# Performance work log

Hardware: AMD Instinct MI355X
Metric: run time of the kernel (lower is better)

The kernel has to match this reference:

```python
import jax, jax.numpy as jnp
import numpy as np

N_KG, N, E, R, H, D_OUT = 50000, 20000, 320000, 8, 4, 64
IN_CH = 256  # 128 kg_emb + 128 ccle projection
HD = H * D_OUT  # 256


def setup_inputs() -> dict:
    key = jax.random.key(0)
    ks = jax.random.split(key, 16)
    nrm = lambda k, shape, s=0.05: jax.random.normal(k, shape, dtype=jnp.float32) * s
    return {
        "kg_emb": nrm(ks[0], (N_KG, 128), 1.0),
        "ccle": nrm(ks[1], (N_KG, 4), 1.0),
        "node_id": jax.random.randint(ks[2], (N,), 0, N_KG),
        "edge_index": jax.random.randint(ks[3], (2, E), 0, N),
        "edge_type": jax.random.randint(ks[4], (E,), 0, R),
        "ccle_w1": nrm(ks[5], (4, 32)), "ccle_b1": jnp.zeros((32,), jnp.float32),
        "ccle_w2": nrm(ks[6], (32, 128)), "ccle_b2": jnp.zeros((128,), jnp.float32),
        "w1": nrm(ks[7], (R, IN_CH, HD)),
        "q1": nrm(ks[8], (HD, H)), "k1": nrm(ks[9], (HD, H)),
        "bias1": jnp.zeros((HD,), jnp.float32),
        "w2": nrm(ks[10], (R, HD, HD)),
        "q2": nrm(ks[11], (HD, H)), "k2": nrm(ks[12], (HD, H)),
        "bias2": jnp.zeros((HD,), jnp.float32),
        "skip_w1": nrm(ks[13], (IN_CH, 256)), "skip_b1": jnp.zeros((256,), jnp.float32),
        "skip_w2": nrm(ks[14], (256, 256)), "skip_b2": jnp.zeros((256,), jnp.float32),
    }


def _segment_softmax(logits, segs, n):
    # numerically stable softmax over variable-size dst-neighborhoods
    m = jax.lax.stop_gradient(jax.ops.segment_max(logits, segs, num_segments=n))
    m = jnp.where(jnp.isfinite(m), m, 0.0)
    e = jnp.exp(logits - m[segs])
    s = jax.ops.segment_sum(e, segs, num_segments=n)
    return e / jnp.maximum(s[segs], 1e-16)


def _rgat(x, edge_index, edge_type, w, q, k, bias, n):
    # PyG RGATConv: additive-self-attention, across-relation, dim=1, concat=True
    # per-relation node transform then per-edge gather == x_e @ w[edge_type]
    xw = jnp.einsum('nd,rdo->rno', x, w)              # [R, N, H*D]
    src, dst = edge_index[0], edge_index[1]
    outj = xw[edge_type, src]                          # [E, H*D] source feats
    outi = xw[edge_type, dst]                          # [E, H*D] target feats
    alpha = jax.nn.leaky_relu(outi @ q + outj @ k, 0.2)  # [E, H]
    alpha = _segment_softmax(alpha, dst, n)
    msg = (outj.reshape(-1, H, D_OUT) * alpha[:, :, None]).reshape(-1, HD)
    return jax.ops.segment_sum(msg, dst, num_segments=n) + bias


def reference(kg_emb, ccle, ccle_w1, ccle_b1, ccle_w2, ccle_b2,
              w1, q1, k1, bias1, w2, q2, k2, bias2,
              skip_w1, skip_b1, skip_w2, skip_b2,
              node_id, edge_index, edge_type):
    lrelu = lambda v: jax.nn.leaky_relu(v, 0.01)  # nn.LeakyReLU default slope
    ccle_out = lrelu(ccle @ ccle_w1 + ccle_b1) @ ccle_w2 + ccle_b2
    x_in = jnp.concatenate([kg_emb[node_id], ccle_out[node_id]], axis=1)  # [N, 256]
    n = x_in.shape[0]
    x = lrelu(_rgat(x_in, edge_index, edge_type, w1, q1, k1, bias1, n))
    # dropout is identity in eval mode
    x = _rgat(x, edge_index, edge_type, w2, q2, k2, bias2, n)
    skip = lrelu(x_in @ skip_w1 + skip_b1) @ skip_w2 + skip_b2
    return lrelu(x + skip)
```

## Files before the change

### kernel.cpp

```cpp
#include <hip/hip_runtime.h>
#include <hip/hip_bf16.h>

typedef __bf16 bf16x8 __attribute__((ext_vector_type(8)));
typedef float  f32x4  __attribute__((ext_vector_type(4)));
typedef float  v2f    __attribute__((ext_vector_type(2)));

#define BUCKET 128

__device__ __forceinline__ void async_cp16(const __bf16* g, __bf16* l) {
    __builtin_amdgcn_global_load_lds(
        (const __attribute__((address_space(1))) void*)g,
        (__attribute__((address_space(3))) void*)l, 16, 0, 0);
}

__global__ __launch_bounds__(256) void preamble_kernel(
    const float* __restrict__ kg_emb, const float* __restrict__ ccle,
    const float* __restrict__ cw1, const float* __restrict__ cb1,
    const float* __restrict__ cw2, const float* __restrict__ cb2,
    const int* __restrict__ node_id, __bf16* __restrict__ x_in, int Nn,
    const float* __restrict__ w1, const float* __restrict__ w2,
    const float* __restrict__ sw1, const float* __restrict__ sw2,
    __bf16* __restrict__ w1t, __bf16* __restrict__ w2t,
    __bf16* __restrict__ sw1t, __bf16* __restrict__ sw2t, int R,
    const float* __restrict__ q1, const float* __restrict__ k1,
    const float* __restrict__ q2, const float* __restrict__ k2,
    __bf16* __restrict__ wqkT1, __bf16* __restrict__ wqkT2,
    const int* __restrict__ ei, const int* __restrict__ et,
    int* __restrict__ cnt, int* __restrict__ cidx, int E,
    int nTrans, int nWqk, int nBx)
{
    __shared__ __align__(16) char sraw[8448];
    const int bid = blockIdx.x;
    const int t = threadIdx.x;

    if (bid < nTrans) {
        __bf16 (*tile)[65] = (__bf16 (*)[65])sraw;
        int zr = bid >> 4, rem = bid & 15;
        int kb = (rem & 3) * 64, nb = (rem >> 2) * 64;
        const float* B; __bf16* Bt;
        if (zr < R)           { B = w1 + (size_t)zr * 65536;       Bt = w1t + (size_t)zr * 65536; }
        else if (zr < 2 * R)  { B = w2 + (size_t)(zr - R) * 65536; Bt = w2t + (size_t)(zr - R) * 65536; }
        else if (zr == 2 * R) { B = sw1;                            Bt = sw1t; }
        else                  { B = sw2;                            Bt = sw2t; }
        for (int idx = t; idx < 4096; idx += 256) {
            int rr = idx >> 6, cc = idx & 63;
            tile[rr][cc] = (__bf16)B[(kb + rr) * 256 + nb + cc];
        }
        __syncthreads();
        for (int idx = t; idx < 4096; idx += 256) {
            int rr = idx >> 6, cc = idx & 63;
            Bt[(nb + rr) * 256 + kb + cc] = tile[cc][rr];
        }
    } else if (bid < nTrans + nWqk) {
        float* qs = (float*)sraw;
        float* ks = qs + 1024;
        int wb = bid - nTrans;
        int zz = wb >> 3, ib = wb & 7;
        int r = zz % R;
        const float* w = (zz < R) ? w1 : w2;
        const float* q = (zz < R) ? q1 : q2;
        const float* k = (zz < R) ? k1 : k2;
        __bf16* wqkT = (zz < R) ? wqkT1 : wqkT2;
        for (int i = t; i < 1024; i += 256) { qs[i] = q[i]; ks[i] = k[i]; }
        __syncthreads();
        int inl = t >> 3, g = t & 7;
        const float* wr = w + (size_t)r * 65536;
        int in = ib * 32 + inl;
        float pq0=0,pq1=0,pq2=0,pq3=0, pk0=0,pk1=0,pk2=0,pk3=0;
        const float* row = wr + in * 256 + g * 32;
        #pragma unroll 8
        for (int oj = 0; oj < 32; oj++) {
            float wv = row[oj];
            int out = g * 32 + oj;
            pq0 += wv * qs[out*4+0]; pq1 += wv * qs[out*4+1];
            pq2 += wv * qs[out*4+2]; pq3 += wv * qs[out*4+3];
            pk0 += wv * ks[out*4+0]; pk1 += wv * ks[out*4+1];
            pk2 += wv * ks[out*4+2]; pk3 += wv * ks[out*4+3];
        }
        #pragma unroll
        for (int d = 4; d >= 1; d >>= 1) {
            pq0 += __shfl_down(pq0, d, 64); pq1 += __shfl_down(pq1, d, 64);
            pq2 += __shfl_down(pq2, d, 64); pq3 += __shfl_down(pq3, d, 64);
            pk0 += __shfl_down(pk0, d, 64); pk1 += __shfl_down(pk1, d, 64);
            pk2 += __shfl_down(pk2, d, 64); pk3 += __shfl_down(pk3, d, 64);
        }
        if (g == 0) {
            wqkT[(r*8+0)*256 + in] = (__bf16)pq0; wqkT[(r*8+1)*256 + in] = (__bf16)pq1;
            wqkT[(r*8+2)*256 + in] = (__bf16)pq2; wqkT[(r*8+3)*256 + in] = (__bf16)pq3;
            wqkT[(r*8+4)*256 + in] = (__bf16)pk0; wqkT[(r*8+5)*256 + in] = (__bf16)pk1;
            wqkT[(r*8+6)*256 + in] = (__bf16)pk2; wqkT[(r*8+7)*256 + in] = (__bf16)pk3;
        }
    } else if (bid < nTrans + nWqk + nBx) {
        float (*h)[32] = (float (*)[32])sraw;
        int bb = bid - nTrans - nWqk;
        int sub = t >> 7;
        int tt  = t & 127;
        int i   = bb * 2 + sub;
        if (i < Nn && tt < 32) {
            int kid = node_id[i];
            float a = 0.f;
            #pragma unroll
            for (int j = 0; j < 4; j++) a += ccle[kid*4 + j] * cw1[j*32 + tt];
            a += cb1[tt];
            h[sub][tt] = a < 0.f ? 0.01f * a : a;
        }
        __syncthreads();
        if (i < Nn) {
            int kid = node_id[i];
            x_in[i*256 + tt] = (__bf16)kg_emb[kid*128 + tt];
            float a = 0.f;
            #pragma unroll
            for (int j = 0; j < 32; j++) a += h[sub][j] * cw2[j*128 + tt];
            a += cb2[tt];
            x_in[i*256 + 128 + tt] = (__bf16)a;
        }
    } else {
        int e = (bid - nTrans - nWqk - nBx) * 256 + t;
        if (e < E) {
            int d = ei[E + e];
            int pos = atomicAdd(&cnt[d], 1);
            if (pos < BUCKET) cidx[(long)d * BUCKET + pos] = (et[e] << 20) | ei[e];
        }
    }
}

__global__ __launch_bounds__(256, 3) void gemm_lds_kernel(
    const __bf16* __restrict__ A, const __bf16* __restrict__ Askip,
    const __bf16* __restrict__ Bt, long bStride, const __bf16* __restrict__ Bskip,
    const __bf16* __restrict__ wqkT,
    unsigned char* __restrict__ C8, long cStride,
    __bf16* __restrict__ Cskip, const float* __restrict__ biasSkip, float slopeSkip,
    float* __restrict__ s_qk,
    int M, int R2, int mb, int nMem, int hasSkip)
{
    __shared__ __bf16 sm[2][8192];
    const int id = blockIdx.x;
    const int xcd = id & 7, slot = id >> 3;
    const int g = xcd + 8 * (slot / nMem);
    const int member = slot % nMem;
    if (g >= mb) return;
    const bool isSqk  = (member == nMem - 1);
    const bool isSkip = hasSkip && !isSqk && (member >= R2);
    const int m0 = g * 128;
    const int n0 = isSkip ? (member - R2) * 128 : ((member < R2) ? (member & 1) * 128 : 0);
    const int z = (member < R2) ? (member >> 1) : 0;
    const __bf16* __restrict__ Ab = isSkip ? Askip : A;
    const __bf16* __restrict__ Bb = isSqk ? wqkT : (isSkip ? Bskip : (Bt + (long)z * bStride));

    const int t = threadIdx.x;
    const int wave = t >> 6, lane = t & 63;
    const int wy = (wave >> 1) * 64, wx = (wave & 1) * 64;
    const int lr = lane & 15, lq = lane >> 4;

    int c0 = wave * 128 + lane;
    int row0 = c0 >> 2, kq0 = ((c0 & 3) ^ ((row0 >> 1) & 3));
    int c1 = c0 + 64;
    int row1 = c1 >> 2, kq1 = ((c1 & 3) ^ ((row1 >> 1) & 3));
    int ar0 = m0 + row0; if (ar0 >= M) ar0 = M - 1;
    int ar1 = m0 + row1; if (ar1 >= M) ar1 = M - 1;
    const long a_g0 = (long)ar0 * 256 + kq0 * 8;
    const long a_g1 = (long)ar1 * 256 + kq1 * 8;
    const long b_g0 = (long)(n0 + row0) * 256 + kq0 * 8;
    const long b_g1 = (long)(n0 + row1) * 256 + kq1 * 8;
    const int lds_w0 = (wave * 128) * 8, lds_w1 = (wave * 128 + 64) * 8;

    int a_lds[4], b_lds[4];
    #pragma unroll
    for (int tm = 0; tm < 4; tm++) {
        int row = wy + tm * 16 + lr;
        a_lds[tm] = (row * 4 + (lq ^ ((row >> 1) & 3))) * 8;
    }
    #pragma unroll
    for (int tn = 0; tn < 4; tn++) {
        int row = wx + tn * 16 + lr;
        b_lds[tn] = 4096 + (row * 4 + (lq ^ ((row >> 1) & 3))) * 8;
    }

    f32x4 acc[4][4];
    #pragma unroll
    for (int a_ = 0; a_ < 4; a_++)
        #pragma unroll
        for (int b_ = 0; b_ < 4; b_++) acc[a_][b_] = (f32x4){0.f, 0.f, 0.f, 0.f};

    async_cp16(Ab + a_g0, &sm[0][lds_w0]);
    async_cp16(Ab + a_g1, &sm[0][lds_w1]);
    async_cp16(Bb + b_g0, &sm[0][4096 + lds_w0]);
    async_cp16(Bb + b_g1, &sm[0][4096 + lds_w1]);

    #pragma unroll
    for (int it = 0; it < 8; it++) {
        const int cur = it & 1;
        __syncthreads();
        if (it < 7) {
            const int k0 = (it + 1) * 32;
            async_cp16(Ab + a_g0 + k0, &sm[cur ^ 1][lds_w0]);
            async_cp16(Ab + a_g1 + k0, &sm[cur ^ 1][lds_w1]);
            async_cp16(Bb + b_g0 + k0, &sm[cur ^ 1][4096 + lds_w0]);
            async_cp16(Bb + b_g1 + k0, &sm[cur ^ 1][4096 + lds_w1]);
        }
        bf16x8 af[4], bfr[4];
        #pragma unroll
        for (int tm = 0; tm < 4; tm++) af[tm]  = *(const bf16x8*)(&sm[cur][a_lds[tm]]);
        #pragma unroll
        for (int tn = 0; tn < 4; tn++) bfr[tn] = *(const bf16x8*)(&sm[cur][b_lds[tn]]);
        #pragma unroll
        for (int tm = 0; tm < 4; tm++)
            #pragma unroll
            for (int tn = 0; tn < 4; tn++)
                acc[tm][tn] = __builtin_amdgcn_mfma_f32_16x16x32_bf16(af[tm], bfr[tn], acc[tm][tn], 0, 0, 0);
    }

    if (isSqk) {
        if (wx == 0) {
            #pragma unroll
            for (int tm = 0; tm < 4; tm++) {
                #pragma unroll
                for (int tn = 0; tn < 4; tn++) {
                    int col = tn * 16 + lr;
                    #pragma unroll
                    for (int ii = 0; ii < 4; ii++) {
                        int rg = m0 + wy + tm * 16 + lq * 4 + ii;
                        if (rg < M) s_qk[(long)rg * 64 + col] = acc[tm][tn][ii];
                    }
                }
            }
        }
    } else if (isSkip) {
        #pragma unroll
        for (int tm = 0; tm < 4; tm++) {
            #pragma unroll
            for (int tn = 0; tn < 4; tn++) {
                int col = n0 + wx + tn * 16 + lr;
                float bcol = biasSkip[col];
                #pragma unroll
                for (int ii = 0; ii < 4; ii++) {
                    int rg = m0 + wy + tm * 16 + lq * 4 + ii;
                    if (rg < M) {
                        float v = acc[tm][tn][ii] + bcol;
                        v = v < 0.f ? v * slopeSkip : v;
                        Cskip[(long)rg * 256 + col] = (__bf16)v;
                    }
                }
            }
        }
    } else {
        unsigned char* __restrict__ Cb = C8 + (long)z * cStride;
        #pragma unroll
        for (int tm = 0; tm < 4; tm++) {
            #pragma unroll
            for (int tn = 0; tn < 4; tn++) {
                int col = n0 + wx + tn * 16 + lr;
                #pragma unroll
                for (int ii = 0; ii < 4; ii++) {
                    int rg = m0 + wy + tm * 16 + lq * 4 + ii;
                    if (rg < M) {
                        float v = acc[tm][tn][ii];
                        int pk = __builtin_amdgcn_cvt_pk_fp8_f32(v, v, 0, false);
                        Cb[(long)rg * 256 + col] = (unsigned char)(pk & 0xFF);
                    }
                }
            }
        }
    }
}

__global__ __launch_bounds__(256) void agg_skip_kernel(
    const unsigned char* __restrict__ XW8, const float* __restrict__ s_qk,
    const int* __restrict__ degArr, const int* __restrict__ cidx,
    const float* __restrict__ bias, __bf16* __restrict__ outb, float slope, int Nn,
    const __bf16* __restrict__ Ask, const __bf16* __restrict__ Bsk,
    __bf16* __restrict__ Csk, const float* __restrict__ biasSk, int nSkip)
{
    extern __shared__ __bf16 smx[];
    if ((int)blockIdx.x < nSkip) {
        const int sb = blockIdx.x;
        const int m0 = (sb >> 1) * 128;
        const int n0 = (sb & 1) * 128;
        const int t = threadIdx.x;
        const int wave = t >> 6, lane = t & 63;
        const int wy = (wave >> 1) * 64, wx = (wave & 1) * 64;
        const int lr = lane & 15, lq = lane >> 4;

        int c0 = wave * 128 + lane;
        int row0 = c0 >> 2, kq0 = ((c0 & 3) ^ ((row0 >> 1) & 3));
        int c1 = c0 + 64;
        int row1 = c1 >> 2, kq1 = ((c1 & 3) ^ ((row1 >> 1) & 3));
        int ar0 = m0 + row0; if (ar0 >= Nn) ar0 = Nn - 1;
        int ar1 = m0 + row1; if (ar1 >= Nn) ar1 = Nn - 1;
        const long a_g0 = (long)ar0 * 256 + kq0 * 8;
        const long a_g1 = (long)ar1 * 256 + kq1 * 8;
        const long b_g0 = (long)(n0 + row0) * 256 + kq0 * 8;
        const long b_g1 = (long)(n0 + row1) * 256 + kq1 * 8;
        const int lds_w0 = (wave * 128) * 8, lds_w1 = (wave * 128 + 64) * 8;

        int a_lds[4], b_lds[4];
        #pragma unroll
        for (int tm = 0; tm < 4; tm++) {
            int row = wy + tm * 16 + lr;
            a_lds[tm] = (row * 4 + (lq ^ ((row >> 1) & 3))) * 8;
        }
        #pragma unroll
        for (int tn = 0; tn < 4; tn++) {
            int row = wx + tn * 16 + lr;
            b_lds[tn] = 4096 + (row * 4 + (lq ^ ((row >> 1) & 3))) * 8;
        }

        f32x4 acc[4][4];
        #pragma unroll
        for (int a_ = 0; a_ < 4; a_++)
            #pragma unroll
            for (int b_ = 0; b_ < 4; b_++) acc[a_][b_] = (f32x4){0.f, 0.f, 0.f, 0.f};

        async_cp16(Ask + a_g0, &smx[lds_w0]);
        async_cp16(Ask + a_g1, &smx[lds_w1]);
        async_cp16(Bsk + b_g0, &smx[4096 + lds_w0]);
        async_cp16(Bsk + b_g1, &smx[4096 + lds_w1]);

        #pragma unroll
        for (int it = 0; it < 8; it++) {
            const int cur = it & 1;
            __syncthreads();
            if (it < 7) {
                const int k0 = (it + 1) * 32;
                async_cp16(Ask + a_g0 + k0, &smx[(cur ^ 1) * 8192 + lds_w0]);
                async_cp16(Ask + a_g1 + k0, &smx[(cur ^ 1) * 8192 + lds_w1]);
                async_cp16(Bsk + b_g0 + k0, &smx[(cur ^ 1) * 8192 + 4096 + lds_w0]);
                async_cp16(Bsk + b_g1 + k0, &smx[(cur ^ 1) * 8192 + 4096 + lds_w1]);
            }
            bf16x8 af[4], bfr[4];
            #pragma unroll
            for (int tm = 0; tm < 4; tm++) af[tm]  = *(const bf16x8*)(&smx[cur * 8192 + a_lds[tm]]);
            #pragma unroll
            for (int tn = 0; tn < 4; tn++) bfr[tn] = *(const bf16x8*)(&smx[cur * 8192 + b_lds[tn]]);
            #pragma unroll
            for (int tm = 0; tm < 4; tm++)
                #pragma unroll
                for (int tn = 0; tn < 4; tn++)
                    acc[tm][tn] = __builtin_amdgcn_mfma_f32_16x16x32_bf16(af[tm], bfr[tn], acc[tm][tn], 0, 0, 0);
        }

        #pragma unroll
        for (int tm = 0; tm < 4; tm++) {
            #pragma unroll
            for (int tn = 0; tn < 4; tn++) {
                int col = n0 + wx + tn * 16 + lr;
                float bcol = biasSk[col];
                #pragma unroll
                for (int ii = 0; ii < 4; ii++) {
                    int rg = m0 + wy + tm * 16 + lq * 4 + ii;
                    if (rg < Nn) Csk[(long)rg * 256 + col] = (__bf16)(acc[tm][tn][ii] + bcol);
                }
            }
        }
        return;
    }

    int* cc_l   = (int*)smx;
    float* p_l  = (float*)((char*)smx + 1024);
    int w = threadIdx.x >> 6;
    int lane = threadIdx.x & 63;
    int i = ((int)blockIdx.x - nSkip) * 4 + w;
    if (i >= Nn) return;
    long base = (long)i * BUCKET;
    int deg = degArr[i]; if (deg > BUCKET) deg = BUCKET;

    int half = lane >> 5;
    int l32 = lane & 31;
    int myh = l32 >> 3;
    int d8 = l32 * 8;

    float4 bv0 = *(const float4*)(bias + d8);
    float4 bv1 = *(const float4*)(bias + d8 + 4);

    float acc[8];
    #pragma unroll
    for (int u = 0; u < 8; u++) acc[u] = 0.f;
    float ss0 = 0.f, ss1 = 0.f, ss2 = 0.f, ss3 = 0.f;

    for (int c0 = 0; c0 < deg; c0 += 64) {
        int e = c0 + lane;
        int cc = 0;
        if (e < deg) cc = cidx[base + e];
        cc_l[w * 64 + lane] = cc;
        int cnt = min(64, deg - c0);

        uint2 xv[8];
        #pragma unroll
        for (int u = 0; u < 8; u++) {
            int cj = cc_l[w * 64 + u * 2 + half];
            int src = cj & 0xFFFFF, et = cj >> 20;
            xv[u] = *(const uint2*)(XW8 + ((long)et * Nn + src) * 256 + d8);
        }

        float p0 = 0.f, p1 = 0.f, p2 = 0.f, p3 = 0.f;
        if (e < deg) {
            int src = cc & 0xFFFFF, et = cc >> 20;
            float4 sqv = *(const float4*)(s_qk + (long)i * 64 + et * 8);
            float4 skv = *(const float4*)(s_qk + (long)src * 64 + et * 8 + 4);
            float l0 = sqv.x + skv.x; l0 = l0 < 0.f ? 0.2f * l0 : l0;
            float l1 = sqv.y + skv.y; l1 = l1 < 0.f ? 0.2f * l1 : l1;
            float l2 = sqv.z + skv.z; l2 = l2 < 0.f ? 0.2f * l2 : l2;
            float l3 = sqv.w + skv.w; l3 = l3 < 0.f ? 0.2f * l3 : l3;
            p0 = __expf(fminf(l0, 40.f)); p1 = __expf(fminf(l1, 40.f));
            p2 = __expf(fminf(l2, 40.f)); p3 = __expf(fminf(l3, 40.f));
        }
// ... 17 lines not shown
            #pragma unroll
            for (int u = 0; u < 8; u++) {
                int srcl = j0 + u * 2 + half;
                float wgt = p_l[(w * 4 + myh) * 64 + srcl];
                uint2 xvu = xv[u];
                v2f f0 = __builtin_amdgcn_cvt_pk_f32_fp8(xvu.x, false);
                v2f f1 = __builtin_amdgcn_cvt_pk_f32_fp8(xvu.x, true);
                v2f f2 = __builtin_amdgcn_cvt_pk_f32_fp8(xvu.y, false);
                v2f f3 = __builtin_amdgcn_cvt_pk_f32_fp8(xvu.y, true);
                acc[0] += wgt * f0.x; acc[1] += wgt * f0.y;
                acc[2] += wgt * f1.x; acc[3] += wgt * f1.y;
                acc[4] += wgt * f2.x; acc[5] += wgt * f2.y;
                acc[6] += wgt * f3.x; acc[7] += wgt * f3.y;
            }
            if (more) {
                #pragma unroll
                for (int u = 0; u < 8; u++) xv[u] = xvn[u];
            }
        }
    }
    #pragma unroll
    for (int u = 0; u < 8; u++) acc[u] += __shfl_xor(acc[u], 32, 64);
    #pragma unroll
    for (int off = 32; off >= 1; off >>= 1) {
        ss0 += __shfl_xor(ss0, off, 64);
        ss1 += __shfl_xor(ss1, off, 64);
        ss2 += __shfl_xor(ss2, off, 64);
        ss3 += __shfl_xor(ss3, off, 64);
    }
    float ssh = (myh & 2) ? ((myh & 1) ? ss3 : ss2) : ((myh & 1) ? ss1 : ss0);
    float inv = 1.f / fmaxf(ssh, 1e-16f);

    float barr[8] = { bv0.x, bv0.y, bv0.z, bv0.w, bv1.x, bv1.y, bv1.z, bv1.w };
    if (half == 0) {
        __bf16 tmp[8];
        #pragma unroll
        for (int u = 0; u < 8; u++) {
            float v = acc[u] * inv + barr[u];
            tmp[u] = (__bf16)(v < 0.f ? slope * v : v);
        }
        *(uint4*)(outb + (long)i * 256 + d8) = *(const uint4*)tmp;
    }
}

__global__ __launch_bounds__(256) void agg_kernel(
    const unsigned char* __restrict__ XW8, const float* __restrict__ s_qk,
    const int* __restrict__ degArr, const int* __restrict__ cidx,
    const float* __restrict__ bias, const __bf16* __restrict__ skipb,
    __bf16* __restrict__ outb, float* __restrict__ outf, float slope, int Nn)
{
    __shared__ int   cc_s[4][64];
    __shared__ float p_s[4][4][64];
    int w = threadIdx.x >> 6;
    int lane = threadIdx.x & 63;
    int i = blockIdx.x * 4 + w;
    if (i >= Nn) return;
    long base = (long)i * BUCKET;
    int deg = degArr[i]; if (deg > BUCKET) deg = BUCKET;

    int half = lane >> 5;
    int l32 = lane & 31;
    int myh = l32 >> 3;
    int d8 = l32 * 8;

    float4 bv0 = *(const float4*)(bias + d8);
    float4 bv1 = *(const float4*)(bias + d8 + 4);
    uint4 skq = make_uint4(0u, 0u, 0u, 0u);
    if (skipb) skq = *(const uint4*)(skipb + (long)i * 256 + d8);

    float acc[8];
    #pragma unroll
    for (int u = 0; u < 8; u++) acc[u] = 0.f;
    float ss0 = 0.f, ss1 = 0.f, ss2 = 0.f, ss3 = 0.f;

    for (int c0 = 0; c0 < deg; c0 += 64) {
        int e = c0 + lane;
        int cc = 0;
        if (e < deg) cc = cidx[base + e];
        cc_s[w][lane] = cc;
        int cnt = min(64, deg - c0);

        uint2 xv[8];
        #pragma unroll
        for (int u = 0; u < 8; u++) {
            int cj = cc_s[w][u * 2 + half];
            int src = cj & 0xFFFFF, et = cj >> 20;
            xv[u] = *(const uint2*)(XW8 + ((long)et * Nn + src) * 256 + d8);
        }

        float p0 = 0.f, p1 = 0.f, p2 = 0.f, p3 = 0.f;
        if (e < deg) {
            int src = cc & 0xFFFFF, et = cc >> 20;
            float4 sqv = *(const float4*)(s_qk + (long)i * 64 + et * 8);
            float4 skv = *(const float4*)(s_qk + (long)src * 64 + et * 8 + 4);
            float l0 = sqv.x + skv.x; l0 = l0 < 0.f ? 0.2f * l0 : l0;
            float l1 = sqv.y + skv.y; l1 = l1 < 0.f ? 0.2f * l1 : l1;
            float l2 = sqv.z + skv.z; l2 = l2 < 0.f ? 0.2f * l2 : l2;
            float l3 = sqv.w + skv.w; l3 = l3 < 0.f ? 0.2f * l3 : l3;
            p0 = __expf(fminf(l0, 40.f)); p1 = __expf(fminf(l1, 40.f));
            p2 = __expf(fminf(l2, 40.f)); p3 = __expf(fminf(l3, 40.f));
        }
        ss0 += p0; ss1 += p1; ss2 += p2; ss3 += p3;
        p_s[w][0][lane] = p0;
        p_s[w][1][lane] = p1;
        p_s[w][2][lane] = p2;
        p_s[w][3][lane] = p3;

        for (int j0 = 0; j0 < cnt; j0 += 16) {
            uint2 xvn[8];
            const bool more = (j0 + 16 < cnt);
            if (more) {
                #pragma unroll
                for (int u = 0; u < 8; u++) {
                    int cj = cc_s[w][j0 + 16 + u * 2 + half];
                    int src = cj & 0xFFFFF, et = cj >> 20;
                    xvn[u] = *(const uint2*)(XW8 + ((long)et * Nn + src) * 256 + d8);
                }
            }
            #pragma unroll
            for (int u = 0; u < 8; u++) {
                int srcl = j0 + u * 2 + half;
                float wgt = p_s[w][myh][srcl];
                uint2 xvu = xv[u];
                v2f f0 = __builtin_amdgcn_cvt_pk_f32_fp8(xvu.x, false);
                v2f f1 = __builtin_amdgcn_cvt_pk_f32_fp8(xvu.x, true);
                v2f f2 = __builtin_amdgcn_cvt_pk_f32_fp8(xvu.y, false);
                v2f f3 = __builtin_amdgcn_cvt_pk_f32_fp8(xvu.y, true);
                acc[0] += wgt * f0.x; acc[1] += wgt * f0.y;
                acc[2] += wgt * f1.x; acc[3] += wgt * f1.y;
                acc[4] += wgt * f2.x; acc[5] += wgt * f2.y;
                acc[6] += wgt * f3.x; acc[7] += wgt * f3.y;
            }
            if (more) {
                #pragma unroll
                for (int u = 0; u < 8; u++) xv[u] = xvn[u];
            }
        }
    }
    #pragma unroll
    for (int u = 0; u < 8; u++) acc[u] += __shfl_xor(acc[u], 32, 64);
    #pragma unroll
    for (int off = 32; off >= 1; off >>= 1) {
        ss0 += __shfl_xor(ss0, off, 64);
        ss1 += __shfl_xor(ss1, off, 64);
        ss2 += __shfl_xor(ss2, off, 64);
        ss3 += __shfl_xor(ss3, off, 64);
    }
    float ssh = (myh & 2) ? ((myh & 1) ? ss3 : ss2) : ((myh & 1) ? ss1 : ss0);
    float inv = 1.f / fmaxf(ssh, 1e-16f);

    float barr[8] = { bv0.x, bv0.y, bv0.z, bv0.w, bv1.x, bv1.y, bv1.z, bv1.w };
    const __bf16* skp = (const __bf16*)&skq;
    float vout[8];
    #pragma unroll
    for (int u = 0; u < 8; u++) {
        float v = acc[u] * inv + barr[u];
        if (skipb) v += (float)skp[u];
        vout[u] = v < 0.f ? slope * v : v;
    }
    if (outb) {
        if (half == 0) {
            __bf16 tmp[8];
            #pragma unroll
            for (int u = 0; u < 8; u++) tmp[u] = (__bf16)vout[u];
            *(uint4*)(outb + (long)i * 256 + d8) = *(const uint4*)tmp;
        }
    } else {
        float4 f4;
        if (half == 0) { f4 = make_float4(vout[0], vout[1], vout[2], vout[3]);
                         *(float4*)(outf + (long)i * 256 + d8) = f4; }
        else           { f4 = make_float4(vout[4], vout[5], vout[6], vout[7]);
                         *(float4*)(outf + (long)i * 256 + d8 + 4) = f4; }
    }
}

extern "C" void kernel_launch(void* const* d_in, const int* in_sizes, int n_in,
                              void* d_out, int out_size, void* d_ws, size_t ws_size,
                              hipStream_t stream)
{
    const float* kg_emb  = (const float*)d_in[0];
    const float* ccle    = (const float*)d_in[1];
    const int*   node_id = (const int*)d_in[2];
    const int*   edge_ix = (const int*)d_in[3];
    const int*   edge_ty = (const int*)d_in[4];
    const float* ccle_w1 = (const float*)d_in[5];
    const float* ccle_b1 = (const float*)d_in[6];
    const float* ccle_w2 = (const float*)d_in[7];
    const float* ccle_b2 = (const float*)d_in[8];
    const float* w1      = (const float*)d_in[9];
    const float* q1      = (const float*)d_in[10];
    const float* k1      = (const float*)d_in[11];
    const float* bias1   = (const float*)d_in[12];
    const float* w2      = (const float*)d_in[13];
    const float* q2      = (const float*)d_in[14];
    const float* k2      = (const float*)d_in[15];
    const float* bias2   = (const float*)d_in[16];
    const float* skip_w1 = (const float*)d_in[17];
    const float* skip_b1 = (const float*)d_in[18];
    const float* skip_w2 = (const float*)d_in[19];
    const float* skip_b2 = (const float*)d_in[20];

    const int Nn = in_sizes[2];
    const int E  = in_sizes[4];
    const int R  = in_sizes[9] / (256 * 256);

    char* p = (char*)d_ws;
    auto alloc = [&](size_t bytes) { char* r = p; p += (bytes + 255) & ~(size_t)255; return r; };
    __bf16* x_in  = (__bf16*)alloc((size_t)Nn * 256 * 2);
    __bf16* x1    = (__bf16*)alloc((size_t)Nn * 256 * 2);
    __bf16* sh    = (__bf16*)alloc((size_t)Nn * 256 * 2);
    __bf16* skipb = (__bf16*)alloc((size_t)Nn * 256 * 2);
    unsigned char* XW8 = (unsigned char*)alloc((size_t)R * Nn * 256);
    float*  s_qk  = (float*)alloc((size_t)Nn * 64 * 4);
    __bf16* wqkT1 = (__bf16*)alloc((size_t)64 * 256 * 2);
    __bf16* wqkT2 = (__bf16*)alloc((size_t)64 * 256 * 2);
    __bf16* w1t   = (__bf16*)alloc((size_t)R * 65536 * 2);
    __bf16* w2t   = (__bf16*)alloc((size_t)R * 65536 * 2);
    __bf16* sw1t  = (__bf16*)alloc((size_t)65536 * 2);
    __bf16* sw2t  = (__bf16*)alloc((size_t)65536 * 2);
    int* cnt  = (int*)alloc((size_t)Nn * 4);
    int* cidx = (int*)alloc((size_t)Nn * BUCKET * 4);

    const int mb = (Nn + 127) / 128;
    const int eb = (E + 255) / 256;
    const int grp = (mb + 7) / 8;
    const int R2 = 2 * R;
    const int gemm1_blocks = 8 * grp * (R2 + 3);
    const int gemm2_blocks = 8 * grp * (R2 + 1);

    const int nTrans = 16 * (2 * R + 2);
    const int nWqk   = 2 * R * 8;
    const int nBx    = (Nn + 1) / 2;
    const int pre_blocks = nTrans + nWqk + nBx + eb;
    const int nSkip2 = 2 * mb;

    (void)hipMemsetAsync(cnt, 0, (size_t)Nn * 4, stream);
    preamble_kernel<<<dim3(pre_blocks), 256, 0, stream>>>(
        kg_emb, ccle, ccle_w1, ccle_b1, ccle_w2, ccle_b2, node_id, x_in, Nn,
        w1, w2, skip_w1, skip_w2, w1t, w2t, sw1t, sw2t, R,
        q1, k1, q2, k2, wqkT1, wqkT2,
        edge_ix, edge_ty, cnt, cidx, E, nTrans, nWqk, nBx);

    gemm_lds_kernel<<<dim3(gemm1_blocks), 256, 0, stream>>>(
        x_in, x_in, w1t, 65536L, sw1t, wqkT1, XW8, (long)Nn * 256, sh, skip_b1, 0.01f,
        s_qk, Nn, R2, mb, R2 + 3, 1);

    agg_skip_kernel<<<dim3(nSkip2 + (Nn + 3) / 4), 256, 32768, stream>>>(
        XW8, s_qk, cnt, cidx, bias1, x1, 0.01f, Nn,
        sh, sw2t, skipb, skip_b2, nSkip2);

    gemm_lds_kernel<<<dim3(gemm2_blocks), 256, 0, stream>>>(
        x1, x1, w2t, 65536L, sw2t, wqkT2, XW8, (long)Nn * 256, skipb, skip_b2, 1.0f,
        s_qk, Nn, R2, mb, R2 + 1, 0);

    agg_kernel<<<dim3((Nn + 3) / 4), 256, 0, stream>>>(
        XW8, s_qk, cnt, cidx, bias2, skipb, nullptr, (float*)d_out, 0.01f, Nn);
}
```

Baseline: 294.5 us.

## Fuse all stages into one persistent kernel with software grid barriers

Replaces the five separate launches (preamble, two GEMMs, two aggregations) with one persistent mega-kernel. Blocks loop over job indices for each stage and are separated by atomic-counter grid barriers. This removes the launch gaps and tail idle time between stages. In exchange every stage now runs with one shared-memory size and register budget, which can lower occupancy for the GEMM (previously launch_bounds 256,3). It also relies on all blocks being co-resident, or the spin barriers can deadlock.

```diff
diff --git a/kernel.cpp b/kernel.cpp
--- a/kernel.cpp
+++ b/kernel.cpp
@@ -13,35 +13,47 @@
         (__attribute__((address_space(3))) void*)l, 16, 0, 0);
 }
 
-__global__ __launch_bounds__(256) void preamble_kernel(
-    const float* __restrict__ kg_emb, const float* __restrict__ ccle,
-    const float* __restrict__ cw1, const float* __restrict__ cb1,
-    const float* __restrict__ cw2, const float* __restrict__ cb2,
-    const int* __restrict__ node_id, __bf16* __restrict__ x_in, int Nn,
-    const float* __restrict__ w1, const float* __restrict__ w2,
-    const float* __restrict__ sw1, const float* __restrict__ sw2,
-    __bf16* __restrict__ w1t, __bf16* __restrict__ w2t,
-    __bf16* __restrict__ sw1t, __bf16* __restrict__ sw2t, int R,
-    const float* __restrict__ q1, const float* __restrict__ k1,
-    const float* __restrict__ q2, const float* __restrict__ k2,
-    __bf16* __restrict__ wqkT1, __bf16* __restrict__ wqkT2,
-    const int* __restrict__ ei, const int* __restrict__ et,
-    int* __restrict__ cnt, int* __restrict__ cidx, int E,
-    int nTrans, int nWqk, int nBx)
+__device__ __forceinline__ void grid_barrier(int* ctr, int nblk) {
+    __syncthreads();
+    if (threadIdx.x == 0) {
+        __threadfence();
+        atomicAdd(ctr, 1);
+        while (atomicAdd(ctr, 0) < nblk) __builtin_amdgcn_s_sleep(2);
+        __threadfence();
+    }
+    __syncthreads();
+}
+
+struct MegaP {
+    const float* kg_emb; const float* ccle;
+    const float* cw1; const float* cb1; const float* cw2; const float* cb2;
+    const int* node_id; __bf16* x_in; int Nn;
+    const float* w1; const float* w2; const float* sw1; const float* sw2;
+    __bf16* w1t; __bf16* w2t; __bf16* sw1t; __bf16* sw2t; int R;
+    const float* q1; const float* k1; const float* q2; const float* k2;
+    __bf16* wqkT1; __bf16* wqkT2;
+    const int* ei; const int* et; int* cnt; int* cidx; int E;
+    int nTrans, nWqk, nBx, nPre;
+    __bf16* x1; __bf16* sh; __bf16* skipb;
+    unsigned char* XW8; float* s_qk;
+    const float* bias1; const float* bias2; const float* skip_b1; const float* skip_b2;
+    float* outf;
+    int R2, mb, g1jobs, g2jobs, nSkip2, agg1jobs, agg2jobs;
+    int* bars; int nBlk;
+};
+
+__device__ void preamble_body(const MegaP& P, int bid, char* sraw)
 {
-    __shared__ __align__(16) char sraw[8448];
-    const int bid = blockIdx.x;
     const int t = threadIdx.x;
-
-    if (bid < nTrans) {
+    if (bid < P.nTrans) {
         __bf16 (*tile)[65] = (__bf16 (*)[65])sraw;
         int zr = bid >> 4, rem = bid & 15;
         int kb = (rem & 3) * 64, nb = (rem >> 2) * 64;
         const float* B; __bf16* Bt;
-        if (zr < R)           { B = w1 + (size_t)zr * 65536;       Bt = w1t + (size_t)zr * 65536; }
-        else if (zr < 2 * R)  { B = w2 + (size_t)(zr - R) * 65536; Bt = w2t + (size_t)(zr - R) * 65536; }
-        else if (zr == 2 * R) { B = sw1;                            Bt = sw1t; }
-        else                  { B = sw2;                            Bt = sw2t; }
+        if (zr < P.R)           { B = P.w1 + (size_t)zr * 65536;         Bt = P.w1t + (size_t)zr * 65536; }
+        else if (zr < 2 * P.R)  { B = P.w2 + (size_t)(zr - P.R) * 65536; Bt = P.w2t + (size_t)(zr - P.R) * 65536; }
+        else if (zr == 2 * P.R) { B = P.sw1;                              Bt = P.sw1t; }
+        else                    { B = P.sw2;                              Bt = P.sw2t; }
         for (int idx = t; idx < 4096; idx += 256) {
             int rr = idx >> 6, cc = idx & 63;
             tile[rr][cc] = (__bf16)B[(kb + rr) * 256 + nb + cc];
@@ -51,16 +63,16 @@
             int rr = idx >> 6, cc = idx & 63;
             Bt[(nb + rr) * 256 + kb + cc] = tile[cc][rr];
         }
-    } else if (bid < nTrans + nWqk) {
+    } else if (bid < P.nTrans + P.nWqk) {
         float* qs = (float*)sraw;
         float* ks = qs + 1024;
-        int wb = bid - nTrans;
+        int wb = bid - P.nTrans;
         int zz = wb >> 3, ib = wb & 7;
-        int r = zz % R;
-        const float* w = (zz < R) ? w1 : w2;
-        const float* q = (zz < R) ? q1 : q2;
-        const float* k = (zz < R) ? k1 : k2;
-        __bf16* wqkT = (zz < R) ? wqkT1 : wqkT2;
+        int r = zz % P.R;
+        const float* w = (zz < P.R) ? P.w1 : P.w2;
+        const float* q = (zz < P.R) ? P.q1 : P.q2;
+        const float* k = (zz < P.R) ? P.k1 : P.k2;
+        __bf16* wqkT = (zz < P.R) ? P.wqkT1 : P.wqkT2;
         for (int i = t; i < 1024; i += 256) { qs[i] = q[i]; ks[i] = k[i]; }
         __syncthreads();
         int inl = t >> 3, g = t & 7;
@@ -90,51 +102,48 @@
             wqkT[(r*8+4)*256 + in] = (__bf16)pk0; wqkT[(r*8+5)*256 + in] = (__bf16)pk1;
             wqkT[(r*8+6)*256 + in] = (__bf16)pk2; wqkT[(r*8+7)*256 + in] = (__bf16)pk3;
         }
-    } else if (bid < nTrans + nWqk + nBx) {
+    } else if (bid < P.nTrans + P.nWqk + P.nBx) {
         float (*h)[32] = (float (*)[32])sraw;
-        int bb = bid - nTrans - nWqk;
+        int bb = bid - P.nTrans - P.nWqk;
         int sub = t >> 7;
         int tt  = t & 127;
         int i   = bb * 2 + sub;
-        if (i < Nn && tt < 32) {
-            int kid = node_id[i];
+        if (i < P.Nn && tt < 32) {
+            int kid = P.node_id[i];
             float a = 0.f;
             #pragma unroll
-            for (int j = 0; j < 4; j++) a += ccle[kid*4 + j] * cw1[j*32 + tt];
-            a += cb1[tt];
+            for (int j = 0; j < 4; j++) a += P.ccle[kid*4 + j] * P.cw1[j*32 + tt];
+            a += P.cb1[tt];
             h[sub][tt] = a < 0.f ? 0.01f * a : a;
         }
         __syncthreads();
-        if (i < Nn) {
-            int kid = node_id[i];
-            x_in[i*256 + tt] = (__bf16)kg_emb[kid*128 + tt];
+        if (i < P.Nn) {
+            int kid = P.node_id[i];
+            P.x_in[i*256 + tt] = (__bf16)P.kg_emb[kid*128 + tt];
             float a = 0.f;
             #pragma unroll
-            for (int j = 0; j < 32; j++) a += h[sub][j] * cw2[j*128 + tt];
-            a += cb2[tt];
-            x_in[i*256 + 128 + tt] = (__bf16)a;
+            for (int j = 0; j < 32; j++) a += h[sub][j] * P.cw2[j*128 + tt];
+            a += P.cb2[tt];
+            P.x_in[i*256 + 128 + tt] = (__bf16)a;
         }
     } else {
-        int e = (bid - nTrans - nWqk - nBx) * 256 + t;
-        if (e < E) {
-            int d = ei[E + e];
-            int pos = atomicAdd(&cnt[d], 1);
-            if (pos < BUCKET) cidx[(long)d * BUCKET + pos] = (et[e] << 20) | ei[e];
-        }
-    }
-}
-
-__global__ __launch_bounds__(256, 3) void gemm_lds_kernel(
-    const __bf16* __restrict__ A, const __bf16* __restrict__ Askip,
+        int e = (bid - P.nTrans - P.nWqk - P.nBx) * 256 + t;
+        if (e < P.E) {
+            int d = P.ei[P.E + e];
+            int pos = atomicAdd(&P.cnt[d], 1);
+            if (pos < BUCKET) P.cidx[(long)d * BUCKET + pos] = (P.et[e] << 20) | P.ei[e];
+        }
+    }
+}
+
+__device__ void gemm_body(
+    int id, const __bf16* __restrict__ A, const __bf16* __restrict__ Askip,
     const __bf16* __restrict__ Bt, long bStride, const __bf16* __restrict__ Bskip,
-    const __bf16* __restrict__ wqkT,
-    unsigned char* __restrict__ C8, long cStride,
+    const __bf16* __restrict__ wqkT, unsigned char* __restrict__ C8, long cStride,
     __bf16* __restrict__ Cskip, const float* __restrict__ biasSkip, float slopeSkip,
-    float* __restrict__ s_qk,
-    int M, int R2, int mb, int nMem, int hasSkip)
+    float* __restrict__ s_qk, int M, int R2, int mb, int nMem, int hasSkip,
+    __bf16* sm)
 {
-    __shared__ __bf16 sm[2][8192];
-    const int id = blockIdx.x;
     const int xcd = id & 7, slot = id >> 3;
     const int g = xcd + 8 * (slot / nMem);
     const int member = slot % nMem;
@@ -182,10 +191,10 @@
         #pragma unroll
         for (int b_ = 0; b_ < 4; b_++) acc[a_][b_] = (f32x4){0.f, 0.f, 0.f, 0.f};
 
-    async_cp16(Ab + a_g0, &sm[0][lds_w0]);
-    async_cp16(Ab + a_g1, &sm[0][lds_w1]);
-    async_cp16(Bb + b_g0, &sm[0][4096 + lds_w0]);
-    async_cp16(Bb + b_g1, &sm[0][4096 + lds_w1]);
+    async_cp16(Ab + a_g0, &sm[lds_w0]);
+    async_cp16(Ab + a_g1, &sm[lds_w1]);
+    async_cp16(Bb + b_g0, &sm[4096 + lds_w0]);
+    async_cp16(Bb + b_g1, &sm[4096 + lds_w1]);
 
     #pragma unroll
     for (int it = 0; it < 8; it++) {
@@ -193,16 +202,16 @@
         __syncthreads();
         if (it < 7) {
             const int k0 = (it + 1) * 32;
-            async_cp16(Ab + a_g0 + k0, &sm[cur ^ 1][lds_w0]);
-            async_cp16(Ab + a_g1 + k0, &sm[cur ^ 1][lds_w1]);
-            async_cp16(Bb + b_g0 + k0, &sm[cur ^ 1][4096 + lds_w0]);
-            async_cp16(Bb + b_g1 + k0, &sm[cur ^ 1][4096 + lds_w1]);
+            async_cp16(Ab + a_g0 + k0, &sm[(cur ^ 1) * 8192 + lds_w0]);
+            async_cp16(Ab + a_g1 + k0, &sm[(cur ^ 1) * 8192 + lds_w1]);
+            async_cp16(Bb + b_g0 + k0, &sm[(cur ^ 1) * 8192 + 4096 + lds_w0]);
+            async_cp16(Bb + b_g1 + k0, &sm[(cur ^ 1) * 8192 + 4096 + lds_w1]);
         }
         bf16x8 af[4], bfr[4];
         #pragma unroll
-        for (int tm = 0; tm < 4; tm++) af[tm]  = *(const bf16x8*)(&sm[cur][a_lds[tm]]);
-        #pragma unroll
-        for (int tn = 0; tn < 4; tn++) bfr[tn] = *(const bf16x8*)(&sm[cur][b_lds[tn]]);
+        for (int tm = 0; tm < 4; tm++) af[tm]  = *(const bf16x8*)(&sm[cur * 8192 + a_lds[tm]]);
+        #pragma unroll
+        for (int tn = 0; tn < 4; tn++) bfr[tn] = *(const bf16x8*)(&sm[cur * 8192 + b_lds[tn]]);
         #pragma unroll
         for (int tm = 0; tm < 4; tm++)
             #pragma unroll
@@ -264,102 +273,102 @@
     }
 }
 
-__global__ __launch_bounds__(256) void agg_skip_kernel(
-    const unsigned char* __restrict__ XW8, const float* __restrict__ s_qk,
+__device__ void skiprider_body(
+    int sb, const __bf16* __restrict__ Ask, const __bf16* __restrict__ Bsk,
+    __bf16* __restrict__ Csk, const float* __restrict__ biasSk, int Nn, __bf16* smx)
+{
+    const int m0 = (sb >> 1) * 128;
+    const int n0 = (sb & 1) * 128;
+    const int t = threadIdx.x;
+    const int wave = t >> 6, lane = t & 63;
+    const int wy = (wave >> 1) * 64, wx = (wave & 1) * 64;
+    const int lr = lane & 15, lq = lane >> 4;
+
+    int c0 = wave * 128 + lane;
+    int row0 = c0 >> 2, kq0 = ((c0 & 3) ^ ((row0 >> 1) & 3));
+    int c1 = c0 + 64;
+    int row1 = c1 >> 2, kq1 = ((c1 & 3) ^ ((row1 >> 1) & 3));
+    int ar0 = m0 + row0; if (ar0 >= Nn) ar0 = Nn - 1;
+    int ar1 = m0 + row1; if (ar1 >= Nn) ar1 = Nn - 1;
+    const long a_g0 = (long)ar0 * 256 + kq0 * 8;
+    const long a_g1 = (long)ar1 * 256 + kq1 * 8;
+    const long b_g0 = (long)(n0 + row0) * 256 + kq0 * 8;
+    const long b_g1 = (long)(n0 + row1) * 256 + kq1 * 8;
+    const int lds_w0 = (wave * 128) * 8, lds_w1 = (wave * 128 + 64) * 8;
+
+    int a_lds[4], b_lds[4];
+    #pragma unroll
+    for (int tm = 0; tm < 4; tm++) {
+        int row = wy + tm * 16 + lr;
+        a_lds[tm] = (row * 4 + (lq ^ ((row >> 1) & 3))) * 8;
+    }
+    #pragma unroll
+    for (int tn = 0; tn < 4; tn++) {
+        int row = wx + tn * 16 + lr;
+        b_lds[tn] = 4096 + (row * 4 + (lq ^ ((row >> 1) & 3))) * 8;
+    }
+
+    f32x4 acc[4][4];
+    #pragma unroll
+    for (int a_ = 0; a_ < 4; a_++)
+        #pragma unroll
+        for (int b_ = 0; b_ < 4; b_++) acc[a_][b_] = (f32x4){0.f, 0.f, 0.f, 0.f};
+
+    async_cp16(Ask + a_g0, &smx[lds_w0]);
+    async_cp16(Ask + a_g1, &smx[lds_w1]);
+    async_cp16(Bsk + b_g0, &smx[4096 + lds_w0]);
+    async_cp16(Bsk + b_g1, &smx[4096 + lds_w1]);
+
+    #pragma unroll
+    for (int it = 0; it < 8; it++) {
+        const int cur = it & 1;
+        __syncthreads();
+        if (it < 7) {
+            const int k0 = (it + 1) * 32;
+            async_cp16(Ask + a_g0 + k0, &smx[(cur ^ 1) * 8192 + lds_w0]);
+            async_cp16(Ask + a_g1 + k0, &smx[(cur ^ 1) * 8192 + lds_w1]);
+            async_cp16(Bsk + b_g0 + k0, &smx[(cur ^ 1) * 8192 + 4096 + lds_w0]);
+            async_cp16(Bsk + b_g1 + k0, &smx[(cur ^ 1) * 8192 + 4096 + lds_w1]);
+        }
+        bf16x8 af[4], bfr[4];
+        #pragma unroll
+        for (int tm = 0; tm < 4; tm++) af[tm]  = *(const bf16x8*)(&smx[cur * 8192 + a_lds[tm]]);
+        #pragma unroll
+        for (int tn = 0; tn < 4; tn++) bfr[tn] = *(const bf16x8*)(&smx[cur * 8192 + b_lds[tn]]);
+        #pragma unroll
+        for (int tm = 0; tm < 4; tm++)
+            #pragma unroll
+            for (int tn = 0; tn < 4; tn++)
+                acc[tm][tn] = __builtin_amdgcn_mfma_f32_16x16x32_bf16(af[tm], bfr[tn], acc[tm][tn], 0, 0, 0);
+    }
+
+    #pragma unroll
+    for (int tm = 0; tm < 4; tm++) {
+        #pragma unroll
+        for (int tn = 0; tn < 4; tn++) {
+            int col = n0 + wx + tn * 16 + lr;
+            float bcol = biasSk[col];
+            #pragma unroll
+            for (int ii = 0; ii < 4; ii++) {
+                int rg = m0 + wy + tm * 16 + lq * 4 + ii;
+                if (rg < Nn) Csk[(long)rg * 256 + col] = (__bf16)(acc[tm][tn][ii] + bcol);
+            }
+        }
+    }
+}
+
+__device__ void agg_body(
+    int job, const unsigned char* __restrict__ XW8, const float* __restrict__ s_qk,
     const int* __restrict__ degArr, const int* __restrict__ cidx,
-    const float* __restrict__ bias, __bf16* __restrict__ outb, float slope, int Nn,
-    const __bf16* __restrict__ Ask, const __bf16* __restrict__ Bsk,
-    __bf16* __restrict__ Csk, const float* __restrict__ biasSk, int nSkip)
+    const float* __restrict__ bias, const __bf16* __restrict__ skipb,
+    __bf16* __restrict__ outb, float* __restrict__ outf, float slope, int Nn,
+    char* smem)
 {
-    extern __shared__ __bf16 smx[];
-    if ((int)blockIdx.x < nSkip) {
-        const int sb = blockIdx.x;
-        const int m0 = (sb >> 1) * 128;
-        const int n0 = (sb & 1) * 128;
-        const int t = threadIdx.x;
-        const int wave = t >> 6, lane = t & 63;
-        const int wy = (wave >> 1) * 64, wx = (wave & 1) * 64;
-        const int lr = lane & 15, lq = lane >> 4;
-
-        int c0 = wave * 128 + lane;
-        int row0 = c0 >> 2, kq0 = ((c0 & 3) ^ ((row0 >> 1) & 3));
-        int c1 = c0 + 64;
-        int row1 = c1 >> 2, kq1 = ((c1 & 3) ^ ((row1 >> 1) & 3));
-        int ar0 = m0 + row0; if (ar0 >= Nn) ar0 = Nn - 1;
-        int ar1 = m0 + row1; if (ar1 >= Nn) ar1 = Nn - 1;
-        const long a_g0 = (long)ar0 * 256 + kq0 * 8;
-        const long a_g1 = (long)ar1 * 256 + kq1 * 8;
-        const long b_g0 = (long)(n0 + row0) * 256 + kq0 * 8;
-        const long b_g1 = (long)(n0 + row1) * 256 + kq1 * 8;
-        const int lds_w0 = (wave * 128) * 8, lds_w1 = (wave * 128 + 64) * 8;
-
-        int a_lds[4], b_lds[4];
-        #pragma unroll
-        for (int tm = 0; tm < 4; tm++) {
-            int row = wy + tm * 16 + lr;
-            a_lds[tm] = (row * 4 + (lq ^ ((row >> 1) & 3))) * 8;
-        }
-        #pragma unroll
-        for (int tn = 0; tn < 4; tn++) {
-            int row = wx + tn * 16 + lr;
-            b_lds[tn] = 4096 + (row * 4 + (lq ^ ((row >> 1) & 3))) * 8;
-        }
-
-        f32x4 acc[4][4];
-        #pragma unroll
-        for (int a_ = 0; a_ < 4; a_++)
-            #pragma unroll
-            for (int b_ = 0; b_ < 4; b_++) acc[a_][b_] = (f32x4){0.f, 0.f, 0.f, 0.f};
-
-        async_cp16(Ask + a_g0, &smx[lds_w0]);
-        async_cp16(Ask + a_g1, &smx[lds_w1]);
-        async_cp16(Bsk + b_g0, &smx[4096 + lds_w0]);
-        async_cp16(Bsk + b_g1, &smx[4096 + lds_w1]);
-
-        #pragma unroll
-        for (int it = 0; it < 8; it++) {
-            const int cur = it & 1;
-            __syncthreads();
-            if (it < 7) {
-                const int k0 = (it + 1) * 32;
-                async_cp16(Ask + a_g0 + k0, &smx[(cur ^ 1) * 8192 + lds_w0]);
-                async_cp16(Ask + a_g1 + k0, &smx[(cur ^ 1) * 8192 + lds_w1]);
-                async_cp16(Bsk + b_g0 + k0, &smx[(cur ^ 1) * 8192 + 4096 + lds_w0]);
-                async_cp16(Bsk + b_g1 + k0, &smx[(cur ^ 1) * 8192 + 4096 + lds_w1]);
-            }
-            bf16x8 af[4], bfr[4];
-            #pragma unroll
-            for (int tm = 0; tm < 4; tm++) af[tm]  = *(const bf16x8*)(&smx[cur * 8192 + a_lds[tm]]);
-            #pragma unroll
-            for (int tn = 0; tn < 4; tn++) bfr[tn] = *(const bf16x8*)(&smx[cur * 8192 + b_lds[tn]]);
-            #pragma unroll
-            for (int tm = 0; tm < 4; tm++)
-                #pragma unroll
-                for (int tn = 0; tn < 4; tn++)
-                    acc[tm][tn] = __builtin_amdgcn_mfma_f32_16x16x32_bf16(af[tm], bfr[tn], acc[tm][tn], 0, 0, 0);
-        }
-
-        #pragma unroll
-        for (int tm = 0; tm < 4; tm++) {
-            #pragma unroll
-            for (int tn = 0; tn < 4; tn++) {
-                int col = n0 + wx + tn * 16 + lr;
-                float bcol = biasSk[col];
-                #pragma unroll
-                for (int ii = 0; ii < 4; ii++) {
-                    int rg = m0 + wy + tm * 16 + lq * 4 + ii;
-                    if (rg < Nn) Csk[(long)rg * 256 + col] = (__bf16)(acc[tm][tn][ii] + bcol);
-                }
-            }
-        }
-        return;
-    }
-
-    int* cc_l   = (int*)smx;
-    float* p_l  = (float*)((char*)smx + 1024);
+    int* cc_l  = (int*)smem;
+    float* p_l = (float*)(smem + 1024);
     int w = threadIdx.x >> 6;
     int lane = threadIdx.x & 63;
-    int i = ((int)blockIdx.x - nSkip) * 4 + w;
+    int i = job * 4 + w;
     if (i >= Nn) return;
     long base = (long)i * BUCKET;
     int deg = degArr[i]; if (deg > BUCKET) deg = BUCKET;
@@ -371,6 +380,8 @@
 
     float4 bv0 = *(const float4*)(bias + d8);
     float4 bv1 = *(const float4*)(bias + d8 + 4);
+    uint4 skq = make_uint4(0u, 0u, 0u, 0u);
+    if (skipb) skq = *(const uint4*)(skipb + (long)i * 256 + d8);
 
     float acc[8];
     #pragma unroll
@@ -454,124 +465,6 @@
     float inv = 1.f / fmaxf(ssh, 1e-16f);
 
     float barr[8] = { bv0.x, bv0.y, bv0.z, bv0.w, bv1.x, bv1.y, bv1.z, bv1.w };
-    if (half == 0) {
-        __bf16 tmp[8];
-        #pragma unroll
-        for (int u = 0; u < 8; u++) {
-            float v = acc[u] * inv + barr[u];
-            tmp[u] = (__bf16)(v < 0.f ? slope * v : v);
-        }
-        *(uint4*)(outb + (long)i * 256 + d8) = *(const uint4*)tmp;
-    }
-}
-
-__global__ __launch_bounds__(256) void agg_kernel(
-    const unsigned char* __restrict__ XW8, const float* __restrict__ s_qk,
-    const int* __restrict__ degArr, const int* __restrict__ cidx,
-    const float* __restrict__ bias, const __bf16* __restrict__ skipb,
-    __bf16* __restrict__ outb, float* __restrict__ outf, float slope, int Nn)
-{
-    __shared__ int   cc_s[4][64];
-    __shared__ float p_s[4][4][64];
-    int w = threadIdx.x >> 6;
-    int lane = threadIdx.x & 63;
-    int i = blockIdx.x * 4 + w;
-    if (i >= Nn) return;
-    long base = (long)i * BUCKET;
-    int deg = degArr[i]; if (deg > BUCKET) deg = BUCKET;
-
-    int half = lane >> 5;
-    int l32 = lane & 31;
-    int myh = l32 >> 3;
-    int d8 = l32 * 8;
-
-    float4 bv0 = *(const float4*)(bias + d8);
-    float4 bv1 = *(const float4*)(bias + d8 + 4);
-    uint4 skq = make_uint4(0u, 0u, 0u, 0u);
-    if (skipb) skq = *(const uint4*)(skipb + (long)i * 256 + d8);
-
-    float acc[8];
-    #pragma unroll
-    for (int u = 0; u < 8; u++) acc[u] = 0.f;
-    float ss0 = 0.f, ss1 = 0.f, ss2 = 0.f, ss3 = 0.f;
-
-    for (int c0 = 0; c0 < deg; c0 += 64) {
-        int e = c0 + lane;
-        int cc = 0;
-        if (e < deg) cc = cidx[base + e];
-        cc_s[w][lane] = cc;
-        int cnt = min(64, deg - c0);
-
-        uint2 xv[8];
-        #pragma unroll
-        for (int u = 0; u < 8; u++) {
-            int cj = cc_s[w][u * 2 + half];
-            int src = cj & 0xFFFFF, et = cj >> 20;
-            xv[u] = *(const uint2*)(XW8 + ((long)et * Nn + src) * 256 + d8);
-        }
-
-        float p0 = 0.f, p1 = 0.f, p2 = 0.f, p3 = 0.f;
-        if (e < deg) {
-            int src = cc & 0xFFFFF, et = cc >> 20;
-            float4 sqv = *(const float4*)(s_qk + (long)i * 64 + et * 8);
-            float4 skv = *(const float4*)(s_qk + (long)src * 64 + et * 8 + 4);
-            float l0 = sqv.x + skv.x; l0 = l0 < 0.f ? 0.2f * l0 : l0;
-            float l1 = sqv.y + skv.y; l1 = l1 < 0.f ? 0.2f * l1 : l1;
-            float l2 = sqv.z + skv.z; l2 = l2 < 0.f ? 0.2f * l2 : l2;
-            float l3 = sqv.w + skv.w; l3 = l3 < 0.f ? 0.2f * l3 : l3;
-            p0 = __expf(fminf(l0, 40.f)); p1 = __expf(fminf(l1, 40.f));
-            p2 = __expf(fminf(l2, 40.f)); p3 = __expf(fminf(l3, 40.f));
-        }
-        ss0 += p0; ss1 += p1; ss2 += p2; ss3 += p3;
-        p_s[w][0][lane] = p0;
-        p_s[w][1][lane] = p1;
-        p_s[w][2][lane] = p2;
-        p_s[w][3][lane] = p3;
-
-        for (int j0 = 0; j0 < cnt; j0 += 16) {
-            uint2 xvn[8];
-            const bool more = (j0 + 16 < cnt);
-            if (more) {
-                #pragma unroll
-                for (int u = 0; u < 8; u++) {
-                    int cj = cc_s[w][j0 + 16 + u * 2 + half];
-                    int src = cj & 0xFFFFF, et = cj >> 20;
-                    xvn[u] = *(const uint2*)(XW8 + ((long)et * Nn + src) * 256 + d8);
-                }
-            }
-            #pragma unroll
-            for (int u = 0; u < 8; u++) {
-                int srcl = j0 + u * 2 + half;
-                float wgt = p_s[w][myh][srcl];
-                uint2 xvu = xv[u];
-                v2f f0 = __builtin_amdgcn_cvt_pk_f32_fp8(xvu.x, false);
-                v2f f1 = __builtin_amdgcn_cvt_pk_f32_fp8(xvu.x, true);
-                v2f f2 = __builtin_amdgcn_cvt_pk_f32_fp8(xvu.y, false);
-                v2f f3 = __builtin_amdgcn_cvt_pk_f32_fp8(xvu.y, true);
-                acc[0] += wgt * f0.x; acc[1] += wgt * f0.y;
-                acc[2] += wgt * f1.x; acc[3] += wgt * f1.y;
-                acc[4] += wgt * f2.x; acc[5] += wgt * f2.y;
-                acc[6] += wgt * f3.x; acc[7] += wgt * f3.y;
-            }
-            if (more) {
-                #pragma unroll
-                for (int u = 0; u < 8; u++) xv[u] = xvn[u];
-            }
-        }
-    }
-    #pragma unroll
-    for (int u = 0; u < 8; u++) acc[u] += __shfl_xor(acc[u], 32, 64);
-    #pragma unroll
-    for (int off = 32; off >= 1; off >>= 1) {
-        ss0 += __shfl_xor(ss0, off, 64);
-        ss1 += __shfl_xor(ss1, off, 64);
-        ss2 += __shfl_xor(ss2, off, 64);
-        ss3 += __shfl_xor(ss3, off, 64);
-    }
-    float ssh = (myh & 2) ? ((myh & 1) ? ss3 : ss2) : ((myh & 1) ? ss1 : ss0);
-    float inv = 1.f / fmaxf(ssh, 1e-16f);
-
-    float barr[8] = { bv0.x, bv0.y, bv0.z, bv0.w, bv1.x, bv1.y, bv1.z, bv1.w };
     const __bf16* skp = (const __bf16*)&skq;
     float vout[8];
     #pragma unroll
@@ -593,6 +486,50 @@
                          *(float4*)(outf + (long)i * 256 + d8) = f4; }
         else           { f4 = make_float4(vout[4], vout[5], vout[6], vout[7]);
                          *(float4*)(outf + (long)i * 256 + d8 + 4) = f4; }
+    }
+}
+
+__global__ __launch_bounds__(256) void mega_kernel(MegaP P)
+{
+    __shared__ __align__(16) char smem[32768];
+    const long cStride = (long)P.Nn * 256;
+
+    for (int j = blockIdx.x; j < P.nPre; j += gridDim.x) {
+        preamble_body(P, j, smem);
+        __syncthreads();
+    }
+    grid_barrier(P.bars + 0, P.nBlk);
+
+    for (int j = blockIdx.x; j < P.g1jobs; j += gridDim.x) {
+        gemm_body(j, P.x_in, P.x_in, P.w1t, 65536L, P.sw1t, P.wqkT1, P.XW8, cStride,
+                  P.sh, P.skip_b1, 0.01f, P.s_qk, P.Nn, P.R2, P.mb, P.R2 + 3, 1,
+                  (__bf16*)smem);
+        __syncthreads();
+    }
+    grid_barrier(P.bars + 1, P.nBlk);
+
+    for (int j = blockIdx.x; j < P.agg1jobs; j += gridDim.x) {
+        if (j < P.nSkip2)
+            skiprider_body(j, P.sh, P.sw2t, P.skipb, P.skip_b2, P.Nn, (__bf16*)smem);
+        else
+            agg_body(j - P.nSkip2, P.XW8, P.s_qk, P.cnt, P.cidx, P.bias1, nullptr,
+                     P.x1, nullptr, 0.01f, P.Nn, smem);
+        __syncthreads();
+    }
+    grid_barrier(P.bars + 2, P.nBlk);
+
+    for (int j = blockIdx.x; j < P.g2jobs; j += gridDim.x) {
+        gemm_body(j, P.x1, P.x1, P.w2t, 65536L, P.sw2t, P.wqkT2, P.XW8, cStride,
+                  P.skipb, P.skip_b2, 1.0f, P.s_qk, P.Nn, P.R2, P.mb, P.R2 + 1, 0,
+                  (__bf16*)smem);
+        __syncthreads();
+    }
+    grid_barrier(P.bars + 3, P.nBlk);
+
+    for (int j = blockIdx.x; j < P.agg2jobs; j += gridDim.x) {
+        agg_body(j, P.XW8, P.s_qk, P.cnt, P.cidx, P.bias2, P.skipb,
+                 nullptr, P.outf, 0.01f, P.Nn, smem);
+        __syncthreads();
     }
 }
 
@@ -642,39 +579,55 @@
     __bf16* sw2t  = (__bf16*)alloc((size_t)65536 * 2);
     int* cnt  = (int*)alloc((size_t)Nn * 4);
     int* cidx = (int*)alloc((size_t)Nn * BUCKET * 4);
+    int* bars = (int*)alloc(256);
 
     const int mb = (Nn + 127) / 128;
     const int eb = (E + 255) / 256;
     const int grp = (mb + 7) / 8;
     const int R2 = 2 * R;
-    const int gemm1_blocks = 8 * grp * (R2 + 3);
-    const int gemm2_blocks = 8 * grp * (R2 + 1);
-
-    const int nTrans = 16 * (2 * R + 2);
-    const int nWqk   = 2 * R * 8;
-    const int nBx    = (Nn + 1) / 2;
-    const int pre_blocks = nTrans + nWqk + nBx + eb;
-    const int nSkip2 = 2 * mb;
+
+    MegaP P;
+    P.kg_emb = kg_emb; P.ccle = ccle;
+    P.cw1 = ccle_w1; P.cb1 = ccle_b1; P.cw2 = ccle_w2; P.cb2 = ccle_b2;
+    P.node_id = node_id; P.x_in = x_in; P.Nn = Nn;
+    P.w1 = w1; P.w2 = w2; P.sw1 = skip_w1; P.sw2 = skip_w2;
+    P.w1t = w1t; P.w2t = w2t; P.sw1t = sw1t; P.sw2t = sw2t; P.R = R;
+    P.q1 = q1; P.k1 = k1; P.q2 = q2; P.k2 = k2;
+    P.wqkT1 = wqkT1; P.wqkT2 = wqkT2;
+    P.ei = edge_ix; P.et = edge_ty; P.cnt = cnt; P.cidx = cidx; P.E = E;
+    P.nTrans = 16 * (2 * R + 2);
+    P.nWqk   = 2 * R * 8;
+    P.nBx    = (Nn + 1) / 2;
+    P.nPre   = P.nTrans + P.nWqk + P.nBx + eb;
+    P.x1 = x1; P.sh = sh; P.skipb = skipb;
+    P.XW8 = XW8; P.s_qk = s_qk;
+    P.bias1 = bias1; P.bias2 = bias2; P.skip_b1 = skip_b1; P.skip_b2 = skip_b2;
+    P.outf = (float*)d_out;
+    P.R2 = R2; P.mb = mb;
+    P.g1jobs = 8 * grp * (R2 + 3);
+    P.g2jobs = 8 * grp * (R2 + 1);
+    P.nSkip2 = 2 * mb;
+    P.agg1jobs = P.nSkip2 + (Nn + 3) / 4;
+    P.agg2jobs = (Nn + 3) / 4;
+    P.bars = bars;
+
+    static int gridBlocks = 0;
+    if (gridBlocks == 0) {
+        int perCU = 0;
+        (void)hipOccupancyMaxActiveBlocksPerMultiprocessor(&perCU, mega_kernel, 256, 0);
+        if (perCU < 1) perCU = 1;
+        if (perCU > 5) perCU = 5;
+        int dev = 0;
+        (void)hipGetDevice(&dev);
+        hipDeviceProp_t prop;
+        (void)hipGetDeviceProperties(&prop, dev);
+        int nCU = prop.multiProcessorCount > 0 ? prop.multiProcessorCount : 256;
+        gridBlocks = (perCU * nCU) & ~7;
+        if (gridBlocks < 256) gridBlocks = 256;
+    }
+    P.nBlk = gridBlocks;
 
     (void)hipMemsetAsync(cnt, 0, (size_t)Nn * 4, stream);
-    preamble_kernel<<<dim3(pre_blocks), 256, 0, stream>>>(
-        kg_emb, ccle, ccle_w1, ccle_b1, ccle_w2, ccle_b2, node_id, x_in, Nn,
-        w1, w2, skip_w1, skip_w2, w1t, w2t, sw1t, sw2t, R,
-        q1, k1, q2, k2, wqkT1, wqkT2,
-        edge_ix, edge_ty, cnt, cidx, E, nTrans, nWqk, nBx);
-
-    gemm_lds_kernel<<<dim3(gemm1_blocks), 256, 0, stream>>>(
-        x_in, x_in, w1t, 65536L, sw1t, wqkT1, XW8, (long)Nn * 256, sh, skip_b1, 0.01f,
-        s_qk, Nn, R2, mb, R2 + 3, 1);
-
-    agg_skip_kernel<<<dim3(nSkip2 + (Nn + 3) / 4), 256, 32768, stream>>>(
-        XW8, s_qk, cnt, cidx, bias1, x1, 0.01f, Nn,
-        sh, sw2t, skipb, skip_b2, nSkip2);
-
-    gemm_lds_kernel<<<dim3(gemm2_blocks), 256, 0, stream>>>(
-        x1, x1, w2t, 65536L, sw2t, wqkT2, XW8, (long)Nn * 256, skipb, skip_b2, 1.0f,
-        s_qk, Nn, R2, mb, R2 + 1, 0);
-
-    agg_kernel<<<dim3((Nn + 3) / 4), 256, 0, stream>>>(
-        XW8, s_qk, cnt, cidx, bias2, skipb, nullptr, (float*)d_out, 0.01f, Nn);
-}
+    (void)hipMemsetAsync(bars, 0, 256, stream);
+    hipLaunchKernelGGL(mega_kernel, dim3(gridBlocks), dim3(256), 0, stream, P);
+}
```

Measured after the change: 620.7 us. +110.7%, slower.
